# Kernel tuning notes

Hardware: AMD Instinct MI355X
Metric: run time of the kernel (lower is better)

The kernel has to match this reference:

```python
import jax, jax.numpy as jnp
import numpy as np

D_MODEL = 1024
N_HEADS = 16
HEAD_DIM = D_MODEL // N_HEADS
ROPE_BASE = 10000.0


def setup_inputs() -> dict:
    key = jax.random.key(0)
    ks = jax.random.split(key, 5)
    B, S = 4, 2048
    bound_qkv = 1.0 / np.sqrt(D_MODEL)
    bound_out = 1.0 / np.sqrt(D_MODEL)
    return {
        "query": jax.random.normal(ks[0], (B, S, D_MODEL), dtype=jnp.float32),
        "W_qkv": jax.random.uniform(ks[1], (3 * D_MODEL, D_MODEL), jnp.float32, -bound_qkv, bound_qkv),
        "b_qkv": jax.random.uniform(ks[2], (3 * D_MODEL,), jnp.float32, -bound_qkv, bound_qkv),
        "W_out": jax.random.uniform(ks[3], (D_MODEL, D_MODEL), jnp.float32, -bound_out, bound_out),
        "b_out": jax.random.uniform(ks[4], (D_MODEL,), jnp.float32, -bound_out, bound_out),
    }


def _rope(x):
    # x: [B, H, S, Dh]; rotate-half RoPE, full rotational fraction
    S, Dh = x.shape[2], x.shape[3]
    half = Dh // 2
    inv_freq = 1.0 / (ROPE_BASE ** (jnp.arange(0, half, dtype=jnp.float32) * 2.0 / Dh))
    ang = jnp.arange(S, dtype=jnp.float32)[:, None] * inv_freq[None, :]  # [S, half]
    cos = jnp.concatenate([jnp.cos(ang), jnp.cos(ang)], axis=-1)  # [S, Dh]
    sin = jnp.concatenate([jnp.sin(ang), jnp.sin(ang)], axis=-1)
    x1, x2 = x[..., :half], x[..., half:]
    rot = jnp.concatenate([-x2, x1], axis=-1)
    return x * cos + rot * sin


def reference(query, W_qkv, b_qkv, W_out, b_out):
    B, S, _ = query.shape
    qkv = query @ W_qkv.T + b_qkv  # [B, S, 3*D]
    qkv = qkv.reshape(B, S, 3, N_HEADS, HEAD_DIM).transpose(2, 0, 3, 1, 4)  # [3, B, H, S, Dh]
    q, k, v = qkv[0], qkv[1], qkv[2]
    q = _rope(q)
    k = _rope(k)
    scale = 1.0 / np.sqrt(HEAD_DIM)
    scores = jnp.einsum("bhsd,bhtd->bhst", q, k) * scale  # [B, H, S, S]
    attn = jax.nn.softmax(scores, axis=-1)
    out = jnp.einsum("bhst,bhtd->bhsd", attn, v)  # [B, H, S, Dh]
    out = out.transpose(0, 2, 1, 3).reshape(B, S, D_MODEL)
    return out @ W_out.T + b_out
```

## Files before the change

### kernel.cpp

```cpp
#include <hip/hip_runtime.h>
#include <math.h>

#define D_MODEL 1024
#define N_HEADS 16
#define HEAD_DIM 64
#define BATCH 4
#define SEQ 2048
#define TOKENS (BATCH * SEQ)

typedef _Float16 f16;
typedef f16 f16x8_t __attribute__((ext_vector_type(8)));
typedef f16 f16x4_t __attribute__((ext_vector_type(4)));
typedef float f32x4_t __attribute__((ext_vector_type(4)));

#define QSCALE 0.18033688011112042f

__device__ __forceinline__ void stage16(const f16* g, f16* l) {
    __builtin_amdgcn_global_load_lds(
        (__attribute__((address_space(1))) void*)g,
        (__attribute__((address_space(3))) void*)l, 16, 0, 0);
}

#define N_X  (TOKENS * D_MODEL / 4)
#define N_WQ (3 * D_MODEL * D_MODEL / 4)
#define N_WO (D_MODEL * D_MODEL / 4)
#define N_CONV (N_X + N_WQ + N_WO)
__global__ void prep_kernel(const float* __restrict__ X,
                            const float* __restrict__ Wq,
                            const float* __restrict__ Wo,
                            f16* __restrict__ Xf, f16* __restrict__ Wqf,
                            f16* __restrict__ Wof,
                            float* __restrict__ cosT, float* __restrict__ sinT) {
    int i = blockIdx.x * blockDim.x + threadIdx.x;
    if (i >= N_CONV) {
        int idx = i - N_CONV;
        int s = idx >> 5;
        int ii = idx & 31;
        double t = (double)(2 * ii) / 64.0;
        double invf = pow(10000.0, -t);
        double ang = (double)s * invf;
        cosT[idx] = (float)cos(ang);
        sinT[idx] = (float)sin(ang);
        return;
    }
    const float* src;
    f16* dst;
    int j;
    if (i < N_X)             { src = X;  dst = Xf;  j = i; }
    else if (i < N_X + N_WQ) { src = Wq; dst = Wqf; j = i - N_X; }
    else                     { src = Wo; dst = Wof; j = i - N_X - N_WQ; }
    float4 x = ((const float4*)src)[j];
    f16x4_t h;
    h[0] = (f16)x.x; h[1] = (f16)x.y; h[2] = (f16)x.z; h[3] = (f16)x.w;
    ((f16x4_t*)dst)[j] = h;
}

__device__ __forceinline__ void gemm_mainloop(
    const f16* __restrict__ A, const f16* __restrict__ B,
    int n0, int c0, f16* As, f16* Bs, f32x4_t acc[4][4]) {
    const int tid = threadIdx.x;
    const int lane = tid & 63;
    const int wave = tid >> 6;
    const int m16 = lane & 15, quad = lane >> 4;
    const int wm = (wave & 1) * 64, wn = (wave >> 1) * 64;

    const int srow = lane >> 3;
    const int scol = (lane & 7) << 3;

#pragma unroll
    for (int i = 0; i < 4; i++)
#pragma unroll
        for (int j = 0; j < 4; j++) acc[i][j] = (f32x4_t){0.f, 0.f, 0.f, 0.f};

    f16* ldsA = As + (wave * 32) * 64;
    f16* ldsB = Bs + (wave * 32) * 64;
    const f16* ga = A + (size_t)(n0 + wave * 32 + srow) * D_MODEL + scol;
    const f16* gb = B + (size_t)(c0 + wave * 32 + srow) * D_MODEL + scol;

    for (int kt = 0; kt < 16; kt++) {
        const int ko = kt * 64;
        __syncthreads();
#pragma unroll
        for (int inst = 0; inst < 4; inst++) {
            stage16(ga + ko + (size_t)(inst * 8) * D_MODEL, ldsA + inst * 8 * 64);
            stage16(gb + ko + (size_t)(inst * 8) * D_MODEL, ldsB + inst * 8 * 64);
        }
        __syncthreads();
#pragma unroll
        for (int kk = 0; kk < 2; kk++) {
            f16x8_t a[4], b[4];
#pragma unroll
            for (int mt = 0; mt < 4; mt++)
                a[mt] = *(const f16x8_t*)&As[(wm + mt * 16 + m16) * 64 + kk * 32 + quad * 8];
#pragma unroll
            for (int nt = 0; nt < 4; nt++)
                b[nt] = *(const f16x8_t*)&Bs[(wn + nt * 16 + m16) * 64 + kk * 32 + quad * 8];
#pragma unroll
            for (int mt = 0; mt < 4; mt++)
#pragma unroll
                for (int nt = 0; nt < 4; nt++)
                    acc[mt][nt] = __builtin_amdgcn_mfma_f32_16x16x32_f16(
                        a[mt], b[nt], acc[mt][nt], 0, 0, 0);
        }
    }
}

__global__ __launch_bounds__(256)
void qkv_gemm_kernel(const f16* __restrict__ Xf, const f16* __restrict__ Wf,
                     const float* __restrict__ bias,
                     f16* __restrict__ Qb, f16* __restrict__ Kb,
                     f16* __restrict__ VbT,
                     const float* __restrict__ cosT, const float* __restrict__ sinT) {
    __shared__ f16 As[128 * 64];
    __shared__ f16 Bs[128 * 64];
    f32x4_t acc[4][4];
    const int n0 = blockIdx.y * 128;
    const int c0 = blockIdx.x * 128;
    gemm_mainloop(Xf, Wf, n0, c0, As, Bs, acc);

    const int lane = threadIdx.x & 63;
    const int wave = threadIdx.x >> 6;
    const int m16 = lane & 15, quad = lane >> 4;
    const int wm = (wave & 1) * 64, wn = (wave >> 1) * 64;

    const int w = c0 >> 10;
    const int hh = ((c0 + wn) & 1023) >> 6;
    const int b = n0 >> 11;

    float bias4[4];
#pragma unroll
    for (int nt = 0; nt < 4; nt++) bias4[nt] = bias[c0 + wn + nt * 16 + m16];

    if (w == 2) {
        f16* vbase = VbT + ((size_t)(b * N_HEADS + hh) * HEAD_DIM) * SEQ;
#pragma unroll
        for (int mt = 0; mt < 4; mt++) {
            const int sb = (n0 + wm + mt * 16 + quad * 4) & (SEQ - 1);
#pragma unroll
            for (int nt = 0; nt < 4; nt++) {
                const int dh = nt * 16 + m16;
                f16x4_t v4;
#pragma unroll
                for (int i = 0; i < 4; i++) v4[i] = (f16)(acc[mt][nt][i] + bias4[nt]);
                *(f16x4_t*)&vbase[(size_t)dh * SEQ + sb] = v4;
            }
        }
        return;
    }

    f16* dst = (w == 0) ? Qb : Kb;
#pragma unroll
    for (int mt = 0; mt < 4; mt++)
#pragma unroll
        for (int i = 0; i < 4; i++) {
            const int n = n0 + wm + mt * 16 + quad * 4 + i;
            const int s = n & (SEQ - 1);
            f16* drow = dst + ((size_t)(b * N_HEADS + hh) * SEQ + s) * HEAD_DIM;
            float vv[4];
#pragma unroll
            for (int nt = 0; nt < 4; nt++) vv[nt] = acc[mt][nt][i] + bias4[nt];
            const float cs0 = cosT[(s << 5) + m16];
            const float sn0 = sinT[(s << 5) + m16];
            const float cs1 = cosT[(s << 5) + 16 + m16];
            const float sn1 = sinT[(s << 5) + 16 + m16];
#pragma unroll
            for (int nt = 0; nt < 4; nt++) {
                const int dh = nt * 16 + m16;
                const float cs = (nt & 1) ? cs1 : cs0;
                const float sn = (nt & 1) ? sn1 : sn0;
                const float part = vv[nt ^ 2];
                float outv = (nt >= 2) ? fmaf(vv[nt], cs, part * sn)
                                       : fmaf(vv[nt], cs, -part * sn);
                if (w == 0) outv *= QSCALE;
                drow[dh] = (f16)outv;
            }
        }
}

__global__ __launch_bounds__(256)
void out_gemm_kernel(const f16* __restrict__ Of, const f16* __restrict__ Wf,
                     const float* __restrict__ bias, float* __restrict__ Cout) {
    __shared__ f16 As[128 * 64];
    __shared__ f16 Bs[128 * 64];
    f32x4_t acc[4][4];
    const int n0 = blockIdx.y * 128;
    const int c0 = blockIdx.x * 128;
    gemm_mainloop(Of, Wf, n0, c0, As, Bs, acc);

    const int lane = threadIdx.x & 63;
    const int wave = threadIdx.x >> 6;
    const int m16 = lane & 15, quad = lane >> 4;
    const int wm = (wave & 1) * 64, wn = (wave >> 1) * 64;

    float bias4[4];
#pragma unroll
    for (int nt = 0; nt < 4; nt++) bias4[nt] = bias[c0 + wn + nt * 16 + m16];

#pragma unroll
    for (int mt = 0; mt < 4; mt++)
#pragma unroll
        for (int i = 0; i < 4; i++) {
            const int n = n0 + wm + mt * 16 + quad * 4 + i;
            float* orow = Cout + (size_t)n * D_MODEL + c0 + wn;
#pragma unroll
            for (int nt = 0; nt < 4; nt++)
                orow[nt * 16 + m16] = acc[mt][nt][i] + bias4[nt];
        }
}

#define KSW(row, g) ((g) ^ ((row) & 7))
#define NT (SEQ / 64)
__global__ __launch_bounds__(256, 2)
void attn_kernel(const f16* __restrict__ Qb, const f16* __restrict__ Kb,
                 const f16* __restrict__ VbT, f16* __restrict__ Of) {
    __shared__ f16 Ks[2][64 * 64];
    __shared__ f16 Vs[2][64 * 64];
    __shared__ f16 Ps[4][64][72];

    const int tid  = threadIdx.x;
    const int lane = tid & 63;
    const int wave = tid >> 6;
    const int m16  = lane & 15;
    const int quad = lane >> 4;

    const int bh = blockIdx.x & 63;
    const int qt = blockIdx.x >> 6;
    const int s0 = qt * 256;

    const f16* Kbase  = Kb + (size_t)bh * SEQ * HEAD_DIM;
    const f16* VtBase = VbT + (size_t)bh * HEAD_DIM * SEQ;

    f16x8_t bq[4][2];
#pragma unroll
    for (int nq = 0; nq < 4; nq++) {
        const f16* qrow = Qb + ((size_t)bh * SEQ + s0 + wave * 64 + nq * 16 + m16)
                          * HEAD_DIM + quad * 8;
        bq[nq][0] = *(const f16x8_t*)(qrow);
        bq[nq][1] = *(const f16x8_t*)(qrow + 32);
    }

    f32x4_t Oc[4][4];
#pragma unroll
    for (int mt = 0; mt < 4; mt++)
#pragma unroll
        for (int nq = 0; nq < 4; nq++) Oc[mt][nq] = (f32x4_t){0.f, 0.f, 0.f, 0.f};
    float sumacc[4] = {0.f, 0.f, 0.f, 0.f};

    const int lrow0 = wave * 16 + (lane >> 3);
    const int lrow1 = lrow0 + 8;
    const int gK0 = lrow0 * HEAD_DIM + KSW(lrow0, lane & 7) * 8;
    const int gK1 = lrow1 * HEAD_DIM + KSW(lrow1, lane & 7) * 8;
    const int gV0 = lrow0 * SEQ + KSW(lrow0, lane & 7) * 8;
    const int gV1 = lrow1 * SEQ + KSW(lrow1, lane & 7) * 8;
    const int lO0 = (wave * 16) * 64;
    const int lO1 = (wave * 16 + 8) * 64;

    stage16(Kbase + gK0, &Ks[0][lO0]);
    stage16(Kbase + gK1, &Ks[0][lO1]);
    stage16(VtBase + gV0, &Vs[0][lO0]);
    stage16(VtBase + gV1, &Vs[0][lO1]);
    asm volatile("s_waitcnt vmcnt(0)" ::: "memory");
    __builtin_amdgcn_s_barrier();
    asm volatile("" ::: "memory");

    for (int kt = 0; kt < NT; kt++) {
        const int cur = kt & 1;

        if (kt + 1 < NT) {
            const f16* kg = Kbase + (size_t)(kt + 1) * 64 * HEAD_DIM;
            const f16* vg = VtBase + (kt + 1) * 64;
            f16* kd = &Ks[cur ^ 1][0];
            f16* vd = &Vs[cur ^ 1][0];
            stage16(kg + gK0, kd + lO0);
            stage16(kg + gK1, kd + lO1);
            stage16(vg + gV0, vd + lO0);
            stage16(vg + gV1, vd + lO1);
        }

        const f16* Kc = &Ks[cur][0];
        const f16* Vc = &Vs[cur][0];

        f32x4_t Sc[4][4];
#pragma unroll
        for (int nt = 0; nt < 4; nt++)
#pragma unroll
            for (int nq = 0; nq < 4; nq++) Sc[nt][nq] = (f32x4_t){0.f, 0.f, 0.f, 0.f};
#pragma unroll
        for (int kki = 0; kki < 2; kki++) {
#pragma unroll
            for (int nt = 0; nt < 4; nt++) {
                const int row = nt * 16 + m16;
                f16x8_t ak = *(const f16x8_t*)&Kc[row * 64 + KSW(row, kki * 4 + quad) * 8];
                __builtin_amdgcn_s_setprio(1);
#pragma unroll
                for (int nq = 0; nq < 4; nq++)
                    Sc[nt][nq] = __builtin_amdgcn_mfma_f32_16x16x32_f16(
                        ak, bq[nq][kki], Sc[nt][nq], 0, 0, 0);
                __builtin_amdgcn_s_setprio(0);
            }
        }

#pragma unroll
        for (int nt = 0; nt < 4; nt++)
#pragma unroll
            for (int nq = 0; nq < 4; nq++) {
                f16x4_t pk4;
#pragma unroll
                for (int i = 0; i < 4; i++) {
                    float p = __builtin_amdgcn_exp2f(Sc[nt][nq][i]);
                    sumacc[nq] += p;
                    pk4[i] = (f16)p;
                }
                *(f16x4_t*)&Ps[wave][nq * 16 + m16][nt * 16 + quad * 4] = pk4;
            }

#pragma unroll
        for (int kki = 0; kki < 2; kki++) {
            f16x8_t bp[4];
#pragma unroll
            for (int nq = 0; nq < 4; nq++)
                bp[nq] = *(const f16x8_t*)&Ps[wave][nq * 16 + m16][kki * 32 + quad * 8];
#pragma unroll
            for (int mt = 0; mt < 4; mt++) {
                const int d = mt * 16 + m16;
                f16x8_t av = *(const f16x8_t*)&Vc[d * 64 + KSW(d, kki * 4 + quad) * 8];
                __builtin_amdgcn_s_setprio(1);
#pragma unroll
                for (int nq = 0; nq < 4; nq++)
                    Oc[mt][nq] = __builtin_amdgcn_mfma_f32_16x16x32_f16(
                        av, bp[nq], Oc[mt][nq], 0, 0, 0);
                __builtin_amdgcn_s_setprio(0);
            }
        }

        asm volatile("s_waitcnt vmcnt(0)" ::: "memory");
        __builtin_amdgcn_s_barrier();
        asm volatile("" ::: "memory");
    }

    const int b = bh >> 4, h = bh & 15;
#pragma unroll
    for (int nq = 0; nq < 4; nq++) {
        float l = sumacc[nq];
        l += __shfl_xor(l, 16);
        l += __shfl_xor(l, 32);
        const float invl = 1.0f / l;
        const int s = s0 + wave * 64 + nq * 16 + m16;
        const size_t off = ((size_t)(b * SEQ + s)) * D_MODEL + h * HEAD_DIM;
#pragma unroll
        for (int mt = 0; mt < 4; mt++) {
            f16x4_t o4;
#pragma unroll
            for (int i = 0; i < 4; i++)
                o4[i] = (f16)(Oc[mt][nq][i] * invl);
            *(f16x4_t*)&Of[off + mt * 16 + quad * 4] = o4;
        }
    }
}

extern "C" void kernel_launch(void* const* d_in, const int* in_sizes, int n_in,
                              void* d_out, int out_size, void* d_ws, size_t ws_size,
                              hipStream_t stream) {
    const float* X    = (const float*)d_in[0];
    const float* Wqkv = (const float*)d_in[1];
    const float* bqkv = (const float*)d_in[2];
    const float* Wout = (const float*)d_in[3];
    const float* bout = (const float*)d_in[4];
    float* out = (float*)d_out;

    char* w8 = (char*)d_ws;
    const size_t MB = 1024 * 1024;
    f16* Xf  = (f16*)(w8);
    f16* Wqf = (f16*)(w8 + 16 * MB);
    f16* Wof = (f16*)(w8 + 22 * MB);
    f16* Qf  = (f16*)(w8 + 24 * MB);
    f16* Kf  = (f16*)(w8 + 40 * MB);
    f16* VfT = (f16*)(w8 + 56 * MB);
    f16* Of  = (f16*)(w8 + 72 * MB);
    float* cosT = (float*)(w8 + 88 * MB);
    float* sinT = cosT + SEQ * 32;

    prep_kernel<<<(N_CONV + SEQ * 32) / 256, 256, 0, stream>>>(
        X, Wqkv, Wout, Xf, Wqf, Wof, cosT, sinT);

    qkv_gemm_kernel<<<dim3(3 * D_MODEL / 128, TOKENS / 128), 256, 0, stream>>>(
        Xf, Wqf, bqkv, Qf, Kf, VfT, cosT, sinT);
    attn_kernel<<<64 * (SEQ / 256), 256, 0, stream>>>(Qf, Kf, VfT, Of);
    out_gemm_kernel<<<dim3(D_MODEL / 128, TOKENS / 128), 256, 0, stream>>>(
        Of, Wof, bout, out);
}
```

Before: 296.9 us.

## Split attention keys across wave pairs, keep P in registers, swizzle GEMM LDS

The attention kernel now uses 128-query tiles. Each pair of waves splits every 64-key tile in half, and the probabilities are fed straight from registers into the PV MFMA instead of round-tripping through an LDS P buffer. To make that register layout work, the V-transposed store in the QKV GEMM permutes token order within each 32-token block. Partial outputs and row sums from the two key halves are combined through LDS at the end. The GEMM mainloop also gets an XOR swizzle on its LDS staging to cut bank conflicts. The trade-off is an extra end-of-kernel reduction, twice as many attention blocks, and a dropped occupancy hint.

```diff
diff --git a/kernel.cpp b/kernel.cpp
--- a/kernel.cpp
+++ b/kernel.cpp
@@ -14,6 +14,8 @@
 typedef float f32x4_t __attribute__((ext_vector_type(4)));
 
 #define QSCALE 0.18033688011112042f
+
+#define KSW(row, g) ((g) ^ ((row) & 7))
 
 __device__ __forceinline__ void stage16(const f16* g, f16* l) {
     __builtin_amdgcn_global_load_lds(
@@ -64,8 +66,8 @@
     const int m16 = lane & 15, quad = lane >> 4;
     const int wm = (wave & 1) * 64, wn = (wave >> 1) * 64;
 
-    const int srow = lane >> 3;
-    const int scol = (lane & 7) << 3;
+    const int srow  = lane >> 3;
+    const int sgran = (lane & 7) ^ srow;
 
 #pragma unroll
     for (int i = 0; i < 4; i++)
@@ -74,8 +76,8 @@
 
     f16* ldsA = As + (wave * 32) * 64;
     f16* ldsB = Bs + (wave * 32) * 64;
-    const f16* ga = A + (size_t)(n0 + wave * 32 + srow) * D_MODEL + scol;
-    const f16* gb = B + (size_t)(c0 + wave * 32 + srow) * D_MODEL + scol;
+    const f16* ga = A + (size_t)(n0 + wave * 32 + srow) * D_MODEL + sgran * 8;
+    const f16* gb = B + (size_t)(c0 + wave * 32 + srow) * D_MODEL + sgran * 8;
 
     for (int kt = 0; kt < 16; kt++) {
         const int ko = kt * 64;
@@ -90,11 +92,15 @@
         for (int kk = 0; kk < 2; kk++) {
             f16x8_t a[4], b[4];
 #pragma unroll
-            for (int mt = 0; mt < 4; mt++)
-                a[mt] = *(const f16x8_t*)&As[(wm + mt * 16 + m16) * 64 + kk * 32 + quad * 8];
-#pragma unroll
-            for (int nt = 0; nt < 4; nt++)
-                b[nt] = *(const f16x8_t*)&Bs[(wn + nt * 16 + m16) * 64 + kk * 32 + quad * 8];
+            for (int mt = 0; mt < 4; mt++) {
+                const int row = wm + mt * 16 + m16;
+                a[mt] = *(const f16x8_t*)&As[row * 64 + KSW(row, kk * 4 + quad) * 8];
+            }
+#pragma unroll
+            for (int nt = 0; nt < 4; nt++) {
+                const int row = wn + nt * 16 + m16;
+                b[nt] = *(const f16x8_t*)&Bs[row * 64 + KSW(row, kk * 4 + quad) * 8];
+            }
 #pragma unroll
             for (int mt = 0; mt < 4; mt++)
 #pragma unroll
@@ -135,7 +141,8 @@
         f16* vbase = VbT + ((size_t)(b * N_HEADS + hh) * HEAD_DIM) * SEQ;
 #pragma unroll
         for (int mt = 0; mt < 4; mt++) {
-            const int sb = (n0 + wm + mt * 16 + quad * 4) & (SEQ - 1);
+            const int sbl = (n0 + wm + (mt >> 1) * 32) & (SEQ - 1);
+            const int sb  = sbl + quad * 8 + (mt & 1) * 4;
 #pragma unroll
             for (int nt = 0; nt < 4; nt++) {
                 const int dh = nt * 16 + m16;
@@ -208,24 +215,25 @@
         }
 }
 
-#define KSW(row, g) ((g) ^ ((row) & 7))
 #define NT (SEQ / 64)
-__global__ __launch_bounds__(256, 2)
+__global__ __launch_bounds__(256)
 void attn_kernel(const f16* __restrict__ Qb, const f16* __restrict__ Kb,
                  const f16* __restrict__ VbT, f16* __restrict__ Of) {
     __shared__ f16 Ks[2][64 * 64];
     __shared__ f16 Vs[2][64 * 64];
-    __shared__ f16 Ps[4][64][72];
+    __shared__ float Lex[2][4][16];
 
     const int tid  = threadIdx.x;
     const int lane = tid & 63;
     const int wave = tid >> 6;
     const int m16  = lane & 15;
     const int quad = lane >> 4;
+    const int kh   = wave & 1;
+    const int qh2  = wave >> 1;
 
     const int bh = blockIdx.x & 63;
     const int qt = blockIdx.x >> 6;
-    const int s0 = qt * 256;
+    const int s0 = qt * 128;
 
     const f16* Kbase  = Kb + (size_t)bh * SEQ * HEAD_DIM;
     const f16* VtBase = VbT + (size_t)bh * HEAD_DIM * SEQ;
@@ -233,7 +241,7 @@
     f16x8_t bq[4][2];
 #pragma unroll
     for (int nq = 0; nq < 4; nq++) {
-        const f16* qrow = Qb + ((size_t)bh * SEQ + s0 + wave * 64 + nq * 16 + m16)
+        const f16* qrow = Qb + ((size_t)bh * SEQ + s0 + qh2 * 64 + nq * 16 + m16)
                           * HEAD_DIM + quad * 8;
         bq[nq][0] = *(const f16x8_t*)(qrow);
         bq[nq][1] = *(const f16x8_t*)(qrow + 32);
@@ -280,16 +288,16 @@
         const f16* Kc = &Ks[cur][0];
         const f16* Vc = &Vs[cur][0];
 
-        f32x4_t Sc[4][4];
-#pragma unroll
-        for (int nt = 0; nt < 4; nt++)
+        f32x4_t Sc[2][4];
+#pragma unroll
+        for (int nt = 0; nt < 2; nt++)
 #pragma unroll
             for (int nq = 0; nq < 4; nq++) Sc[nt][nq] = (f32x4_t){0.f, 0.f, 0.f, 0.f};
 #pragma unroll
         for (int kki = 0; kki < 2; kki++) {
 #pragma unroll
-            for (int nt = 0; nt < 4; nt++) {
-                const int row = nt * 16 + m16;
+            for (int nt = 0; nt < 2; nt++) {
+                const int row = kh * 32 + nt * 16 + m16;
                 f16x8_t ak = *(const f16x8_t*)&Kc[row * 64 + KSW(row, kki * 4 + quad) * 8];
                 __builtin_amdgcn_s_setprio(1);
 #pragma unroll
@@ -300,37 +308,28 @@
             }
         }
 
-#pragma unroll
-        for (int nt = 0; nt < 4; nt++)
-#pragma unroll
-            for (int nq = 0; nq < 4; nq++) {
-                f16x4_t pk4;
+        f16x8_t bp[4];
+#pragma unroll
+        for (int nq = 0; nq < 4; nq++)
+#pragma unroll
+            for (int nt = 0; nt < 2; nt++)
 #pragma unroll
                 for (int i = 0; i < 4; i++) {
                     float p = __builtin_amdgcn_exp2f(Sc[nt][nq][i]);
                     sumacc[nq] += p;
-                    pk4[i] = (f16)p;
+                    bp[nq][nt * 4 + i] = (f16)p;
                 }
-                *(f16x4_t*)&Ps[wave][nq * 16 + m16][nt * 16 + quad * 4] = pk4;
-            }
-
-#pragma unroll
-        for (int kki = 0; kki < 2; kki++) {
-            f16x8_t bp[4];
+
+#pragma unroll
+        for (int mt = 0; mt < 4; mt++) {
+            const int d = mt * 16 + m16;
+            f16x8_t av = *(const f16x8_t*)&Vc[d * 64 + KSW(d, kh * 4 + quad) * 8];
+            __builtin_amdgcn_s_setprio(1);
 #pragma unroll
             for (int nq = 0; nq < 4; nq++)
-                bp[nq] = *(const f16x8_t*)&Ps[wave][nq * 16 + m16][kki * 32 + quad * 8];
-#pragma unroll
-            for (int mt = 0; mt < 4; mt++) {
-                const int d = mt * 16 + m16;
-                f16x8_t av = *(const f16x8_t*)&Vc[d * 64 + KSW(d, kki * 4 + quad) * 8];
-                __builtin_amdgcn_s_setprio(1);
-#pragma unroll
-                for (int nq = 0; nq < 4; nq++)
-                    Oc[mt][nq] = __builtin_amdgcn_mfma_f32_16x16x32_f16(
-                        av, bp[nq], Oc[mt][nq], 0, 0, 0);
-                __builtin_amdgcn_s_setprio(0);
-            }
+                Oc[mt][nq] = __builtin_amdgcn_mfma_f32_16x16x32_f16(
+                    av, bp[nq], Oc[mt][nq], 0, 0, 0);
+            __builtin_amdgcn_s_setprio(0);
         }
 
         asm volatile("s_waitcnt vmcnt(0)" ::: "memory");
@@ -338,22 +337,44 @@
         asm volatile("" ::: "memory");
     }
 
-    const int b = bh >> 4, h = bh & 15;
+    float lred[4];
 #pragma unroll
     for (int nq = 0; nq < 4; nq++) {
         float l = sumacc[nq];
         l += __shfl_xor(l, 16);
         l += __shfl_xor(l, 32);
-        const float invl = 1.0f / l;
-        const int s = s0 + wave * 64 + nq * 16 + m16;
-        const size_t off = ((size_t)(b * SEQ + s)) * D_MODEL + h * HEAD_DIM;
-#pragma unroll
-        for (int mt = 0; mt < 4; mt++) {
-            f16x4_t o4;
-#pragma unroll
-            for (int i = 0; i < 4; i++)
-                o4[i] = (f16)(Oc[mt][nq][i] * invl);
-            *(f16x4_t*)&Of[off + mt * 16 + quad * 4] = o4;
+        lred[nq] = l;
+    }
+
+    float* R = (qh2 == 0) ? (float*)&Ks[0][0] : (float*)&Vs[0][0];
+
+    if (kh == 1) {
+#pragma unroll
+        for (int mt = 0; mt < 4; mt++)
+#pragma unroll
+            for (int nq = 0; nq < 4; nq++)
+                *(f32x4_t*)&R[(nq * 16 + m16) * 64 + mt * 16 + quad * 4] = Oc[mt][nq];
+        if (quad == 0)
+#pragma unroll
+            for (int nq = 0; nq < 4; nq++) Lex[qh2][nq][m16] = lred[nq];
+    }
+    __syncthreads();
+    if (kh == 0) {
+        const int b = bh >> 4, h = bh & 15;
+#pragma unroll
+        for (int nq = 0; nq < 4; nq++) {
+            const float invl = 1.0f / (lred[nq] + Lex[qh2][nq][m16]);
+            const int s = s0 + qh2 * 64 + nq * 16 + m16;
+            const size_t off = ((size_t)(b * SEQ + s)) * D_MODEL + h * HEAD_DIM;
+#pragma unroll
+            for (int mt = 0; mt < 4; mt++) {
+                f32x4_t o = *(const f32x4_t*)&R[(nq * 16 + m16) * 64 + mt * 16 + quad * 4];
+                f16x4_t o4;
+#pragma unroll
+                for (int i = 0; i < 4; i++)
+                    o4[i] = (f16)((Oc[mt][nq][i] + o[i]) * invl);
+                *(f16x4_t*)&Of[off + mt * 16 + quad * 4] = o4;
+            }
         }
     }
 }
@@ -385,7 +406,7 @@
 
     qkv_gemm_kernel<<<dim3(3 * D_MODEL / 128, TOKENS / 128), 256, 0, stream>>>(
         Xf, Wqf, bqkv, Qf, Kf, VfT, cosT, sinT);
-    attn_kernel<<<64 * (SEQ / 256), 256, 0, stream>>>(Qf, Kf, VfT, Of);
+    attn_kernel<<<64 * (SEQ / 128), 256, 0, stream>>>(Qf, Kf, VfT, Of);
     out_gemm_kernel<<<dim3(D_MODEL / 128, TOKENS / 128), 256, 0, stream>>>(
         Of, Wof, bout, out);
 }
```

After: 290.0 us. 1.02x faster.
